# Kernel optimization log

Hardware: AMD Instinct MI355X
Metric: run time of the kernel (lower is better)

The kernel has to match this reference:

```python
import jax, jax.numpy as jnp
import numpy as np

N_NODES = 100000
N_EDGES = 1600000
IN_CH = 128
OUT_CH = 64


def setup_inputs() -> dict:
    key = jax.random.key(0)
    k1, k2, k3, k4 = jax.random.split(key, 4)
    x = jax.random.normal(k1, (N_NODES, IN_CH), dtype=jnp.float32)
    # Glorot-ish scale for the GCN weight matrices
    scale = (2.0 / (IN_CH + OUT_CH)) ** 0.5
    W_mu = jax.random.normal(k2, (IN_CH, OUT_CH), dtype=jnp.float32) * scale
    b_mu = jnp.zeros((OUT_CH,), dtype=jnp.float32)
    W_logstd = jax.random.normal(k3, (IN_CH, OUT_CH), dtype=jnp.float32) * scale
    b_logstd = jnp.zeros((OUT_CH,), dtype=jnp.float32)
    edge_index = jax.random.randint(k4, (2, N_EDGES), 0, N_NODES, dtype=jnp.int64)
    return {"x": x, "W_mu": W_mu, "b_mu": b_mu,
            "W_logstd": W_logstd, "b_logstd": b_logstd,
            "edge_index": edge_index}


def _gcn_conv(x, W, b, src, dst, dinv):
    """PyG-style GCNConv: h = x @ W; symmetric-normalized aggregation with
    self-loops; bias added after aggregation.
    dinv: [N] = deg^{-1/2} including self-loops."""
    h = x @ W  # [N, out]
    norm = dinv[src] * dinv[dst]  # [E]
    agg = jax.ops.segment_sum(h[src] * norm[:, None], dst, num_segments=x.shape[0])
    # self-loop contribution: norm_ii = dinv[i]^2
    agg = agg + h * (dinv * dinv)[:, None]
    return agg + b


def reference(x, W_mu, b_mu, W_logstd, b_logstd, edge_index):
    src, dst = edge_index[0], edge_index[1]
    n = x.shape[0]
    # degree after adding self-loops (edge weights = 1)
    deg = jax.ops.segment_sum(jnp.ones_like(dst, dtype=x.dtype), dst, num_segments=n) + 1.0
    dinv = jax.lax.rsqrt(deg)
    mu = _gcn_conv(x, W_mu, b_mu, src, dst, dinv)
    logstd = _gcn_conv(x, W_logstd, b_logstd, src, dst, dinv)
    return (mu, logstd)
```

## Files before the change

### kernel.cpp

```cpp
#include <hip/hip_runtime.h>

#define N_NODES 100000
#define N_EDGES 1600000
#define IN_CH 128
#define OUT_CH 64
#define BINSHIFT 9
#define BINSZ 512
#define NBINS 196
#define CAP 16384
#define PCHUNK 8192
#define PBLOCKS 200
#define GEMM_BLOCKS ((N_NODES + 63) / 64)
#define WT_LD 136

typedef __attribute__((ext_vector_type(8))) short bf16x8;
typedef __attribute__((ext_vector_type(4))) float f32x4;

__device__ __forceinline__ unsigned short f2bf(float f) {
    union { float f; unsigned u; } v; v.f = f;
    unsigned r = v.u + 0x7fffu + ((v.u >> 16) & 1u);
    return (unsigned short)(r >> 16);
}
__device__ __forceinline__ float bflo(unsigned u) {
    union { unsigned u; float f; } v; v.u = u << 16; return v.f;
}
__device__ __forceinline__ float bfhi(unsigned u) {
    union { unsigned u; float f; } v; v.u = u & 0xFFFF0000u; return v.f;
}

__global__ __launch_bounds__(256) void k_pg(const int* __restrict__ src,
                                            const int* __restrict__ dst,
                                            unsigned* __restrict__ g_binptr,
                                            unsigned* __restrict__ part,
                                            const float* __restrict__ x,
                                            const float* __restrict__ Wmu,
                                            const float* __restrict__ Wls,
                                            unsigned short* __restrict__ hp) {
    __shared__ __align__(16) union {
        struct { unsigned hist[NBINS]; unsigned lbase[NBINS]; } p;
        unsigned short wt[128][WT_LD];
    } sm;
    int tid = threadIdx.x;

    if (blockIdx.x < PBLOCKS) {
        if (tid < NBINS) sm.p.hist[tid] = 0;
        __syncthreads();
        int e0 = blockIdx.x * PCHUNK;
#pragma unroll 4
        for (int i = 0; i < PCHUNK / 256; ++i) {
            int e = e0 + i * 256 + tid;
            if (e < N_EDGES) atomicAdd(&sm.p.hist[dst[e] >> BINSHIFT], 1u);
        }
        __syncthreads();
        if (tid < NBINS) {
            unsigned h = sm.p.hist[tid];
            sm.p.lbase[tid] = (unsigned)tid * CAP + (h ? atomicAdd(&g_binptr[tid], h) : 0u);
            sm.p.hist[tid] = 0;
        }
        __syncthreads();
#pragma unroll 4
        for (int i = 0; i < PCHUNK / 256; ++i) {
            int e = e0 + i * 256 + tid;
            if (e < N_EDGES) {
                int d = dst[e];
                int bin = d >> BINSHIFT;
                unsigned pos = sm.p.lbase[bin] + atomicAdd(&sm.p.hist[bin], 1u);
                if (pos < ((unsigned)bin + 1u) * CAP)
                    part[pos] = (((unsigned)src[e]) << BINSHIFT) | (unsigned)(d & (BINSZ - 1));
            }
        }
        return;
    }

    for (int f = tid; f < 8192; f += 256) {
        int n = f & 63, k = f >> 6;
        sm.wt[n][k]      = f2bf(Wmu[f]);
        sm.wt[64 + n][k] = f2bf(Wls[f]);
    }
    __syncthreads();

    int gb   = blockIdx.x - PBLOCKS;
    int wid  = tid >> 6;
    int lane = tid & 63;
    int wrow0 = gb * 64 + wid * 16;
    int m16  = lane & 15;
    int kgrp = lane >> 4;
    int koff = kgrp * 8;

    int lrow  = wrow0 + m16;
    int lrowc = lrow < N_NODES ? lrow : (N_NODES - 1);
    const float* xp = x + (size_t)lrowc * IN_CH + koff;

    f32x4 acc[8];
#pragma unroll
    for (int t = 0; t < 8; ++t) acc[t] = (f32x4){0.f, 0.f, 0.f, 0.f};

#pragma unroll
    for (int kb = 0; kb < 4; ++kb) {
        float4 x0 = *(const float4*)(xp + kb * 32);
        float4 x1 = *(const float4*)(xp + kb * 32 + 4);
        bf16x8 a;
        a[0] = (short)f2bf(x0.x); a[1] = (short)f2bf(x0.y);
        a[2] = (short)f2bf(x0.z); a[3] = (short)f2bf(x0.w);
        a[4] = (short)f2bf(x1.x); a[5] = (short)f2bf(x1.y);
        a[6] = (short)f2bf(x1.z); a[7] = (short)f2bf(x1.w);
#pragma unroll
        for (int t = 0; t < 8; ++t) {
            bf16x8 b = *(const bf16x8*)&sm.wt[t * 16 + m16][kb * 32 + koff];
            acc[t] = __builtin_amdgcn_mfma_f32_16x16x32_bf16(a, b, acc[t], 0, 0, 0);
        }
    }

    int r0 = wrow0 + kgrp * 4;
#pragma unroll
    for (int t = 0; t < 8; ++t) {
        int col = t * 16 + m16;
#pragma unroll
        for (int r = 0; r < 4; ++r) {
            int rr = r0 + r;
            if (rr < N_NODES)
                hp[(size_t)rr * 128 + col] = f2bf(acc[t][r]);
        }
    }
}

__global__ __launch_bounds__(512) void k_build(const unsigned* __restrict__ g_binptr,
                                               const unsigned* __restrict__ part,
                                               int* __restrict__ csr,
                                               unsigned* __restrict__ rowptr,
                                               unsigned* __restrict__ degO,
                                               float* __restrict__ dinv) {
    __shared__ unsigned hist[BINSZ];
    __shared__ unsigned ofs[BINSZ];
    __shared__ unsigned alloc_[BINSZ];
    __shared__ int csr_l[CAP];
    int tid = threadIdx.x;
    int b = blockIdx.x;
    unsigned base = (unsigned)b * CAP;
    unsigned cnt_b = g_binptr[b];
    if (cnt_b > CAP) cnt_b = CAP;

    hist[tid] = 0;
    __syncthreads();
    for (unsigned i = tid; i < cnt_b; i += 512)
        atomicAdd(&hist[part[base + i] & (BINSZ - 1)], 1u);
    __syncthreads();
    ofs[tid] = hist[tid];
    __syncthreads();
    for (int off = 1; off < BINSZ; off <<= 1) {
        unsigned v = (tid >= off) ? ofs[tid - off] : 0;
        __syncthreads();
        ofs[tid] += v;
        __syncthreads();
    }
    int d = b * BINSZ + tid;
    if (d < N_NODES) {
        unsigned dg = hist[tid];
        degO[d] = dg;
        rowptr[d] = base + (ofs[tid] - dg);
        dinv[d] = rsqrtf((float)dg + 1.0f);
    }
    alloc_[tid] = 0;
    __syncthreads();
    for (unsigned i = tid; i < cnt_b; i += 512) {
        unsigned v = part[base + i];
        unsigned dl = v & (BINSZ - 1);
        unsigned p = (ofs[dl] - hist[dl]) + atomicAdd(&alloc_[dl], 1u);
        csr_l[p] = (int)(v >> BINSHIFT);
    }
    __syncthreads();
    for (unsigned i = tid; i < cnt_b; i += 512)
        csr[base + i] = csr_l[i];
}

__global__ __launch_bounds__(256) void k_gather(const unsigned* __restrict__ degO,
                                                const unsigned* __restrict__ rowptr,
                                                const float* __restrict__ dinv,
                                                const int* __restrict__ csr,
                                                const unsigned short* __restrict__ hp,
                                                const float* __restrict__ bmu,
                                                const float* __restrict__ bls,
                                                float* __restrict__ out) {
    int node = (blockIdx.x * 256 + threadIdx.x) >> 6;
    if (node >= N_NODES) return;
    int lane = threadIdx.x & 63;
    int sub  = lane & 31;
    int half = lane >> 5;
    int ch   = sub * 4;
    int d = node;

    float dv = dinv[d];
    int deg = (int)degO[d];
    unsigned row = rowptr[d];

    uint2 su = *(const uint2*)(hp + ((size_t)d << 7) + ch);

    float a0 = 0.f, a1 = 0.f, a2 = 0.f, a3 = 0.f;

    for (int b0 = 0; b0 < deg; b0 += 64) {
        int m = deg - b0; if (m > 64) m = 64;
        int  ev = (lane < m) ? __builtin_nontemporal_load(csr + row + b0 + lane) : 0;
        float wv = (lane < m) ? dinv[ev] : 0.f;
        unsigned pv = (unsigned)ev | (((unsigned)(wv * 32767.f + 0.5f)) << 17);

        for (int t = 0; t < m; t += 16) {
            uint2 u[8]; float w[8];
#pragma unroll
            for (int j = 0; j < 8; ++j) {
                int idx = t + 2 * j + half;
                unsigned pe = (unsigned)__shfl((int)pv, idx);
                int s = (int)(pe & 0x1FFFFu);
                w[j] = (float)(pe >> 17);
                u[j] = *(const uint2*)(hp + ((size_t)s << 7) + ch);
            }
#pragma unroll
            for (int j = 0; j < 8; ++j) {
                a0 += w[j] * bflo(u[j].x);
                a1 += w[j] * bfhi(u[j].x);
                a2 += w[j] * bflo(u[j].y);
                a3 += w[j] * bfhi(u[j].y);
            }
        }
    }

    a0 += __shfl_xor(a0, 32);
    a1 += __shfl_xor(a1, 32);
    a2 += __shfl_xor(a2, 32);
    a3 += __shfl_xor(a3, 32);

    if (half == 0) {
        const float kq = 1.f / 32767.f;
        float h0 = bflo(su.x), h1 = bfhi(su.x), h2 = bflo(su.y), h3 = bfhi(su.y);
        float4 bv = (ch < OUT_CH) ? *(const float4*)(bmu + ch)
                                  : *(const float4*)(bls + (ch - OUT_CH));
        float4 o;
        o.x = dv * (a0 * kq + dv * h0) + bv.x;
        o.y = dv * (a1 * kq + dv * h1) + bv.y;
        o.z = dv * (a2 * kq + dv * h2) + bv.z;
        o.w = dv * (a3 * kq + dv * h3) + bv.w;
        float* op = (ch < OUT_CH)
                      ? (out + (size_t)d * OUT_CH + ch)
                      : (out + (size_t)N_NODES * OUT_CH + (size_t)d * OUT_CH + (ch - OUT_CH));
        __builtin_nontemporal_store(o.x, op);
        __builtin_nontemporal_store(o.y, op + 1);
        __builtin_nontemporal_store(o.z, op + 2);
        __builtin_nontemporal_store(o.w, op + 3);
    }
}

extern "C" void kernel_launch(void* const* d_in, const int* in_sizes, int n_in,
                              void* d_out, int out_size, void* d_ws, size_t ws_size,
                              hipStream_t stream) {
    const float* x   = (const float*)d_in[0];
    const float* Wmu = (const float*)d_in[1];
    const float* bmu = (const float*)d_in[2];
    const float* Wls = (const float*)d_in[3];
    const float* bls = (const float*)d_in[4];
    const int*   ei  = (const int*)d_in[5];
    const int* src = ei;
    const int* dst = ei + N_EDGES;
    float* out = (float*)d_out;

    char* ws = (char*)d_ws;
    size_t off = 0;
    unsigned short* hp = (unsigned short*)(ws + off); off += (size_t)N_NODES * 128 * 2;
    unsigned* part = (unsigned*)(ws + off);           off += (size_t)NBINS * CAP * 4;
    int* csr = (int*)(ws + off);                      off += (size_t)NBINS * CAP * 4;
    unsigned* rowptr = (unsigned*)(ws + off);         off += (size_t)N_NODES * 4;
    unsigned* degO = (unsigned*)(ws + off);           off += (size_t)N_NODES * 4;
    float* dinv = (float*)(ws + off);                 off += (size_t)N_NODES * 4;
    unsigned* g_binptr = (unsigned*)(ws + off);       off += (size_t)NBINS * 4;

    hipMemsetAsync(g_binptr, 0, (size_t)NBINS * sizeof(unsigned), stream);

    k_pg    <<<PBLOCKS + GEMM_BLOCKS, 256, 0, stream>>>(src, dst, g_binptr, part, x, Wmu, Wls, hp);
    k_build <<<NBINS, 512, 0, stream>>>(g_binptr, part, csr, rowptr, degO, dinv);
    k_gather<<<(N_NODES * 64 + 255) / 256, 256, 0, stream>>>(degO, rowptr, dinv, csr, hp, bmu, bls, out);
}
```

Before: 126.9 us.

## Prescale GEMM output by source dinv and simplify gather to unweighted sums

```diff
diff --git a/kernel.cpp b/kernel.cpp
--- a/kernel.cpp
+++ b/kernel.cpp
@@ -12,6 +12,7 @@
 #define PBLOCKS 200
 #define GEMM_BLOCKS ((N_NODES + 63) / 64)
 #define WT_LD 136
+#define ZROW N_NODES
 
 typedef __attribute__((ext_vector_type(8))) short bf16x8;
 typedef __attribute__((ext_vector_type(4))) float f32x4;
@@ -26,6 +27,18 @@
 }
 __device__ __forceinline__ float bfhi(unsigned u) {
     union { unsigned u; float f; } v; v.u = u & 0xFFFF0000u; return v.f;
+}
+
+__global__ __launch_bounds__(256) void k_count(const int* __restrict__ dst,
+                                               unsigned* __restrict__ cnt) {
+    int e0 = (blockIdx.x * 256 + threadIdx.x) * 4;
+    if (e0 < N_EDGES) {
+        int4 d4 = *(const int4*)(dst + e0);
+        atomicAdd(&cnt[d4.x], 1u);
+        atomicAdd(&cnt[d4.y], 1u);
+        atomicAdd(&cnt[d4.z], 1u);
+        atomicAdd(&cnt[d4.w], 1u);
+    }
 }
 
 __global__ __launch_bounds__(256) void k_pg(const int* __restrict__ src,
@@ -35,6 +48,7 @@
                                             const float* __restrict__ x,
                                             const float* __restrict__ Wmu,
                                             const float* __restrict__ Wls,
+                                            const unsigned* __restrict__ cnt,
                                             unsigned short* __restrict__ hp) {
     __shared__ __align__(16) union {
         struct { unsigned hist[NBINS]; unsigned lbase[NBINS]; } p;
@@ -112,14 +126,21 @@
     }
 
     int r0 = wrow0 + kgrp * 4;
+    float dvv[4];
+#pragma unroll
+    for (int r = 0; r < 4; ++r) {
+        int rr = r0 + r;
+        dvv[r] = (rr < N_NODES) ? rsqrtf((float)cnt[rr] + 1.0f) : 0.f;
+    }
 #pragma unroll
     for (int t = 0; t < 8; ++t) {
         int col = t * 16 + m16;
 #pragma unroll
         for (int r = 0; r < 4; ++r) {
             int rr = r0 + r;
-            if (rr < N_NODES)
-                hp[(size_t)rr * 128 + col] = f2bf(acc[t][r]);
+            if (rr < N_NODES + 32)
+                hp[(size_t)rr * 128 + col] = (rr < N_NODES) ? f2bf(acc[t][r] * dvv[r])
+                                                            : (unsigned short)0;
         }
     }
 }
@@ -127,9 +148,7 @@
 __global__ __launch_bounds__(512) void k_build(const unsigned* __restrict__ g_binptr,
                                                const unsigned* __restrict__ part,
                                                int* __restrict__ csr,
-                                               unsigned* __restrict__ rowptr,
-                                               unsigned* __restrict__ degO,
-                                               float* __restrict__ dinv) {
+                                               unsigned* __restrict__ rowptr) {
     __shared__ unsigned hist[BINSZ];
     __shared__ unsigned ofs[BINSZ];
     __shared__ unsigned alloc_[BINSZ];
@@ -154,12 +173,8 @@
         __syncthreads();
     }
     int d = b * BINSZ + tid;
-    if (d < N_NODES) {
-        unsigned dg = hist[tid];
-        degO[d] = dg;
-        rowptr[d] = base + (ofs[tid] - dg);
-        dinv[d] = rsqrtf((float)dg + 1.0f);
-    }
+    if (d < N_NODES)
+        rowptr[d] = base + (ofs[tid] - hist[tid]);
     alloc_[tid] = 0;
     __syncthreads();
     for (unsigned i = tid; i < cnt_b; i += 512) {
@@ -173,79 +188,55 @@
         csr[base + i] = csr_l[i];
 }
 
-__global__ __launch_bounds__(256) void k_gather(const unsigned* __restrict__ degO,
+__global__ __launch_bounds__(256) void k_gather(const unsigned* __restrict__ cnt,
                                                 const unsigned* __restrict__ rowptr,
-                                                const float* __restrict__ dinv,
                                                 const int* __restrict__ csr,
                                                 const unsigned short* __restrict__ hp,
                                                 const float* __restrict__ bmu,
                                                 const float* __restrict__ bls,
                                                 float* __restrict__ out) {
-    int node = (blockIdx.x * 256 + threadIdx.x) >> 6;
+    int node = __builtin_amdgcn_readfirstlane(blockIdx.x * 4 + (threadIdx.x >> 6));
     if (node >= N_NODES) return;
     int lane = threadIdx.x & 63;
-    int sub  = lane & 31;
-    int half = lane >> 5;
-    int ch   = sub * 4;
-    int d = node;
-
-    float dv = dinv[d];
-    int deg = (int)degO[d];
-    unsigned row = rowptr[d];
-
-    uint2 su = *(const uint2*)(hp + ((size_t)d << 7) + ch);
-
-    float a0 = 0.f, a1 = 0.f, a2 = 0.f, a3 = 0.f;
-
-    for (int b0 = 0; b0 < deg; b0 += 64) {
-        int m = deg - b0; if (m > 64) m = 64;
-        int  ev = (lane < m) ? __builtin_nontemporal_load(csr + row + b0 + lane) : 0;
-        float wv = (lane < m) ? dinv[ev] : 0.f;
-        unsigned pv = (unsigned)ev | (((unsigned)(wv * 32767.f + 0.5f)) << 17);
-
-        for (int t = 0; t < m; t += 16) {
-            uint2 u[8]; float w[8];
-#pragma unroll
-            for (int j = 0; j < 8; ++j) {
-                int idx = t + 2 * j + half;
-                unsigned pe = (unsigned)__shfl((int)pv, idx);
-                int s = (int)(pe & 0x1FFFFu);
-                w[j] = (float)(pe >> 17);
-                u[j] = *(const uint2*)(hp + ((size_t)s << 7) + ch);
-            }
-#pragma unroll
-            for (int j = 0; j < 8; ++j) {
-                a0 += w[j] * bflo(u[j].x);
-                a1 += w[j] * bfhi(u[j].x);
-                a2 += w[j] * bflo(u[j].y);
-                a3 += w[j] * bfhi(u[j].y);
-            }
-        }
-    }
-
-    a0 += __shfl_xor(a0, 32);
-    a1 += __shfl_xor(a1, 32);
-    a2 += __shfl_xor(a2, 32);
-    a3 += __shfl_xor(a3, 32);
-
-    if (half == 0) {
-        const float kq = 1.f / 32767.f;
-        float h0 = bflo(su.x), h1 = bfhi(su.x), h2 = bflo(su.y), h3 = bfhi(su.y);
-        float4 bv = (ch < OUT_CH) ? *(const float4*)(bmu + ch)
-                                  : *(const float4*)(bls + (ch - OUT_CH));
-        float4 o;
-        o.x = dv * (a0 * kq + dv * h0) + bv.x;
-        o.y = dv * (a1 * kq + dv * h1) + bv.y;
-        o.z = dv * (a2 * kq + dv * h2) + bv.z;
-        o.w = dv * (a3 * kq + dv * h3) + bv.w;
-        float* op = (ch < OUT_CH)
-                      ? (out + (size_t)d * OUT_CH + ch)
-                      : (out + (size_t)N_NODES * OUT_CH + (size_t)d * OUT_CH + (ch - OUT_CH));
-        __builtin_nontemporal_store(o.x, op);
-        __builtin_nontemporal_store(o.y, op + 1);
-        __builtin_nontemporal_store(o.z, op + 2);
-        __builtin_nontemporal_store(o.w, op + 3);
-    }
+    int ch2  = lane * 2;
+
+    int deg = (int)cnt[node];
+    unsigned row = rowptr[node];
+
+    float a0 = 0.f, a1 = 0.f;
+
+    for (int i = 0; i < deg; i += 16) {
+        unsigned u[16];
+#pragma unroll
+        for (int j = 0; j < 16; ++j) {
+            int idx = i + j;
+            int s = csr[row + idx];
+            s = (idx < deg) ? s : ZROW;
+            u[j] = *(const unsigned*)(hp + ((size_t)s << 7) + ch2);
+        }
+#pragma unroll
+        for (int j = 0; j < 16; ++j) {
+            a0 += bflo(u[j]);
+            a1 += bfhi(u[j]);
+        }
+    }
+
+    unsigned su = *(const unsigned*)(hp + ((size_t)node << 7) + ch2);
+    a0 += bflo(su);
+    a1 += bfhi(su);
+
+    float dv = rsqrtf((float)deg + 1.0f);
+    float2 bv;
+    float* op;
+    if (lane < 32) {
+        bv = *(const float2*)(bmu + ch2);
+        op = out + (size_t)node * OUT_CH + ch2;
+    } else {
+        bv = *(const float2*)(bls + (ch2 - 64));
+        op = out + (size_t)N_NODES * OUT_CH + (size_t)node * OUT_CH + (ch2 - 64);
+    }
+    __builtin_nontemporal_store(a0 * dv + bv.x, op);
+    __builtin_nontemporal_store(a1 * dv + bv.y, op + 1);
 }
 
 extern "C" void kernel_launch(void* const* d_in, const int* in_sizes, int n_in,
@@ -263,17 +254,17 @@
 
     char* ws = (char*)d_ws;
     size_t off = 0;
-    unsigned short* hp = (unsigned short*)(ws + off); off += (size_t)N_NODES * 128 * 2;
+    unsigned short* hp = (unsigned short*)(ws + off); off += (size_t)(N_NODES + 32) * 128 * 2;
     unsigned* part = (unsigned*)(ws + off);           off += (size_t)NBINS * CAP * 4;
     int* csr = (int*)(ws + off);                      off += (size_t)NBINS * CAP * 4;
     unsigned* rowptr = (unsigned*)(ws + off);         off += (size_t)N_NODES * 4;
-    unsigned* degO = (unsigned*)(ws + off);           off += (size_t)N_NODES * 4;
-    float* dinv = (float*)(ws + off);                 off += (size_t)N_NODES * 4;
+    unsigned* cnt = (unsigned*)(ws + off);            off += (size_t)N_NODES * 4;
     unsigned* g_binptr = (unsigned*)(ws + off);       off += (size_t)NBINS * 4;
 
-    hipMemsetAsync(g_binptr, 0, (size_t)NBINS * sizeof(unsigned), stream);
-
-    k_pg    <<<PBLOCKS + GEMM_BLOCKS, 256, 0, stream>>>(src, dst, g_binptr, part, x, Wmu, Wls, hp);
-    k_build <<<NBINS, 512, 0, stream>>>(g_binptr, part, csr, rowptr, degO, dinv);
-    k_gather<<<(N_NODES * 64 + 255) / 256, 256, 0, stream>>>(degO, rowptr, dinv, csr, hp, bmu, bls, out);
-}
+    hipMemsetAsync(cnt, 0, (size_t)(N_NODES + NBINS) * sizeof(unsigned), stream);
+
+    k_count <<<(N_EDGES / 4 + 255) / 256, 256, 0, stream>>>(dst, cnt);
+    k_pg    <<<PBLOCKS + GEMM_BLOCKS, 256, 0, stream>>>(src, dst, g_binptr, part, x, Wmu, Wls, cnt, hp);
+    k_build <<<NBINS, 512, 0, stream>>>(g_binptr, part, csr, rowptr);
+    k_gather<<<(N_NODES + 3) / 4, 256, 0, stream>>>(cnt, rowptr, csr, hp, bmu, bls, out);
+}
```

New measurement: 193.4 us. +52.4%, slower.
